# Optimization experiments

Hardware: AMD Instinct MI355X
Metric: run time of the kernel (lower is better)

Reference implementation:

```python
import jax, jax.numpy as jnp
import numpy as np

B, H, S, D = 4, 16, 4096, 64

def setup_inputs() -> dict:
    key = jax.random.key(0)
    kq, kk, kv = jax.random.split(key, 3)
    q = jax.random.normal(kq, (B, H, S, D), dtype=jnp.float32)
    k = jax.random.normal(kk, (B, H, S, D), dtype=jnp.float32)
    v = jax.random.normal(kv, (B, H, S, D), dtype=jnp.float32)
    return {"q": q, "k": k, "v": v}

def reference(q, k, v):
    # Original: (q @ k^T) @ v with score [B,H,S,S].
    # Mathematically identical reassociation: q @ (k^T @ v),
    # state kv has shape [B,H,D,D] -> avoids the SxS intermediate.
    kv = jnp.einsum('bhsd,bhse->bhde', k, v)  # [B,H,D,D]
    out = jnp.einsum('bhsd,bhde->bhse', q, kv)  # [B,H,S,D]
    return out
```

## Files before the change

### kernel.cpp

```cpp
#include <hip/hip_runtime.h>

#define BH  64
#define SEQ 4096
#define DH  64
#define NCHUNK 16
#define CROWS  (SEQ / NCHUNK)
#define KSTEPS (CROWS / 32)

typedef __attribute__((ext_vector_type(8))) short bf16x8v;
typedef __attribute__((ext_vector_type(4))) float f32x4v;

__device__ __forceinline__ short f2bf(float x) {
  unsigned u = __float_as_uint(x);
  return (short)((u + 0x7FFFu + ((u >> 16) & 1u)) >> 16);
}

__global__ __launch_bounds__(256, 4) void kv_partial_kernel(
    const float* __restrict__ k, const float* __restrict__ v,
    float* __restrict__ partial) {
  const int t = threadIdx.x;
  const int bh = blockIdx.x >> 4;
  const int chunk = blockIdx.x & (NCHUNK - 1);

  const int l  = t & 63;
  const int w  = t >> 6;
  const int lg = l >> 4;
  const int ln = l & 15;
  const int d0 = (w & 1) * 32;
  const int e0 = (w >> 1) * 32;

  const size_t sb = (size_t)bh * SEQ * DH + (size_t)chunk * CROWS * DH;
  const float* kp0 = k + sb + (size_t)(lg * 8) * DH + d0 + ln;
  const float* kp1 = kp0 + 16;
  const float* vp0 = v + sb + (size_t)(lg * 8) * DH + e0 + ln;
  const float* vp1 = vp0 + 16;

  f32x4v acc00 = {0.f, 0.f, 0.f, 0.f};
  f32x4v acc01 = acc00, acc10 = acc00, acc11 = acc00;

  float ck0[8], ck1[8], cv0[8], cv1[8];
#pragma unroll
  for (int j = 0; j < 8; ++j) {
    ck0[j] = kp0[j * DH]; ck1[j] = kp1[j * DH];
    cv0[j] = vp0[j * DH]; cv1[j] = vp1[j * DH];
  }

  for (int ks = 0; ks < KSTEPS; ++ks) {
    float nk0[8], nk1[8], nv0[8], nv1[8];
    if (ks + 1 < KSTEPS) {
      const size_t off = (size_t)(ks + 1) * 32 * DH;
#pragma unroll
      for (int j = 0; j < 8; ++j) {
        nk0[j] = kp0[off + j * DH]; nk1[j] = kp1[off + j * DH];
        nv0[j] = vp0[off + j * DH]; nv1[j] = vp1[off + j * DH];
      }
    }

    bf16x8v a0, a1, b0, b1;
#pragma unroll
    for (int j = 0; j < 8; ++j) {
      a0[j] = f2bf(ck0[j]); a1[j] = f2bf(ck1[j]);
      b0[j] = f2bf(cv0[j]); b1[j] = f2bf(cv1[j]);
    }

    acc00 = __builtin_amdgcn_mfma_f32_16x16x32_bf16(a0, b0, acc00, 0, 0, 0);
    acc01 = __builtin_amdgcn_mfma_f32_16x16x32_bf16(a0, b1, acc01, 0, 0, 0);
    acc10 = __builtin_amdgcn_mfma_f32_16x16x32_bf16(a1, b0, acc10, 0, 0, 0);
    acc11 = __builtin_amdgcn_mfma_f32_16x16x32_bf16(a1, b1, acc11, 0, 0, 0);

    if (ks + 1 < KSTEPS) {
#pragma unroll
      for (int j = 0; j < 8; ++j) {
        ck0[j] = nk0[j]; ck1[j] = nk1[j];
        cv0[j] = nv0[j]; cv1[j] = nv1[j];
      }
    }
  }

  float* pb = partial + (size_t)blockIdx.x * (DH * DH);
  const int rbase = lg * 4;
#pragma unroll
  for (int r = 0; r < 4; ++r) {
    pb[(d0 +  0 + rbase + r) * 64 + e0 +  0 + ln] = acc00[r];
    pb[(d0 +  0 + rbase + r) * 64 + e0 + 16 + ln] = acc01[r];
    pb[(d0 + 16 + rbase + r) * 64 + e0 +  0 + ln] = acc10[r];
    pb[(d0 + 16 + rbase + r) * 64 + e0 + 16 + ln] = acc11[r];
  }
}

__global__ __launch_bounds__(256) void kv_reduce_kernel(
    const float* __restrict__ partial, float* __restrict__ kvf) {
  const int gid = blockIdx.x * 256 + threadIdx.x;
  const int bh = gid >> 10;
  const int idx = gid & 1023;
  float4 s = {0.f, 0.f, 0.f, 0.f};
  for (int c = 0; c < NCHUNK; ++c) {
    const float4* p = (const float4*)(partial + ((size_t)bh * NCHUNK + c) * (DH * DH));
    float4 x = p[idx];
    s.x += x.x; s.y += x.y; s.z += x.z; s.w += x.w;
  }
  ((float4*)kvf)[gid] = s;
}

__global__ __launch_bounds__(256) void out_kernel(
    const float* __restrict__ q, const float* __restrict__ kvf,
    float* __restrict__ out) {
  const int t = threadIdx.x;
  const int bh = blockIdx.x >> 6;
  const int rb = blockIdx.x & 63;
  const int row = rb * 64 + (t >> 2);
  const int c0 = (t & 3) * 16;

  __shared__ float kv_lds[64 * 64];

  const float4* gkv4 = (const float4*)(kvf + (size_t)bh * (DH * DH));
  float4* kv4 = (float4*)kv_lds;
#pragma unroll
  for (int j = 0; j < 4; ++j) kv4[t + j * 256] = gkv4[t + j * 256];

  const float* qrow = q + (size_t)bh * SEQ * DH + (size_t)row * DH;
  float4 qv[16];
#pragma unroll
  for (int i = 0; i < 16; ++i) qv[i] = *(const float4*)&qrow[i * 4];

  __syncthreads();

  float acc[16];
#pragma unroll
  for (int j = 0; j < 16; ++j) acc[j] = 0.f;

#pragma unroll
  for (int dc = 0; dc < 16; ++dc) {
    float qs[4] = {qv[dc].x, qv[dc].y, qv[dc].z, qv[dc].w};
#pragma unroll
    for (int dd = 0; dd < 4; ++dd) {
      const float* kr = &kv_lds[(dc * 4 + dd) * 64 + c0];
      float4 k0 = *(const float4*)&kr[0];
      float4 k1 = *(const float4*)&kr[4];
      float4 k2 = *(const float4*)&kr[8];
      float4 k3 = *(const float4*)&kr[12];
      const float qsv = qs[dd];
      acc[0]  += qsv * k0.x; acc[1]  += qsv * k0.y;
      acc[2]  += qsv * k0.z; acc[3]  += qsv * k0.w;
      acc[4]  += qsv * k1.x; acc[5]  += qsv * k1.y;
      acc[6]  += qsv * k1.z; acc[7]  += qsv * k1.w;
      acc[8]  += qsv * k2.x; acc[9]  += qsv * k2.y;
      acc[10] += qsv * k2.z; acc[11] += qsv * k2.w;
      acc[12] += qsv * k3.x; acc[13] += qsv * k3.y;
      acc[14] += qsv * k3.z; acc[15] += qsv * k3.w;
    }
  }

  float* ob = out + (size_t)bh * SEQ * DH + (size_t)row * DH + c0;
#pragma unroll
  for (int j = 0; j < 4; ++j) {
    float4 w = {acc[4 * j + 0], acc[4 * j + 1], acc[4 * j + 2], acc[4 * j + 3]};
    *(float4*)&ob[4 * j] = w;
  }
}

extern "C" void kernel_launch(void* const* d_in, const int* in_sizes, int n_in,
                              void* d_out, int out_size, void* d_ws, size_t ws_size,
                              hipStream_t stream) {
  const float* q = (const float*)d_in[0];
  const float* k = (const float*)d_in[1];
  const float* v = (const float*)d_in[2];
  float* out = (float*)d_out;

  float* kvf = (float*)d_ws;
  float* partial = kvf + (size_t)BH * DH * DH;

  hipLaunchKernelGGL(kv_partial_kernel, dim3(BH * NCHUNK), dim3(256), 0, stream,
                     k, v, partial);
  hipLaunchKernelGGL(kv_reduce_kernel, dim3(256), dim3(256), 0, stream,
                     partial, kvf);
  hipLaunchKernelGGL(out_kernel, dim3(BH * 64), dim3(256), 0, stream,
                     q, kvf, out);
}
```

Baseline: 76.03 us.

## Stage K/V tiles through LDS with direct global-to-LDS loads, double-buffered

The partial K^T V kernel now copies each 32-row K and V tile into shared memory with 16-byte global_load_lds instructions and double buffering. Operands for the MFMA are then read from LDS, replacing per-lane strided scalar global loads held in registers. The goal is wider, coalesced global accesses and lower register pressure. In exchange it adds 32KB of LDS per block, which may limit occupancy, plus a barrier every iteration.

```diff
diff --git a/kernel.cpp b/kernel.cpp
--- a/kernel.cpp
+++ b/kernel.cpp
@@ -5,7 +5,7 @@
 #define DH  64
 #define NCHUNK 16
 #define CROWS  (SEQ / NCHUNK)
-#define KSTEPS (CROWS / 32)
+#define NT     (CROWS / 32)
 
 typedef __attribute__((ext_vector_type(8))) short bf16x8v;
 typedef __attribute__((ext_vector_type(4))) float f32x4v;
@@ -13,6 +13,12 @@
 __device__ __forceinline__ short f2bf(float x) {
   unsigned u = __float_as_uint(x);
   return (short)((u + 0x7FFFu + ((u >> 16) & 1u)) >> 16);
+}
+
+__device__ __forceinline__ void gload_lds16(const float* g, float* l) {
+  __builtin_amdgcn_global_load_lds(
+      (const __attribute__((address_space(1))) void*)g,
+      (__attribute__((address_space(3))) void*)l, 16, 0, 0);
 }
 
 __global__ __launch_bounds__(256, 4) void kv_partial_kernel(
@@ -29,38 +35,45 @@
   const int d0 = (w & 1) * 32;
   const int e0 = (w >> 1) * 32;
 
-  const size_t sb = (size_t)bh * SEQ * DH + (size_t)chunk * CROWS * DH;
-  const float* kp0 = k + sb + (size_t)(lg * 8) * DH + d0 + ln;
-  const float* kp1 = kp0 + 16;
-  const float* vp0 = v + sb + (size_t)(lg * 8) * DH + e0 + ln;
-  const float* vp1 = vp0 + 16;
+  const float* kb = k + (size_t)bh * SEQ * DH + (size_t)chunk * CROWS * DH;
+  const float* vb = v + (size_t)bh * SEQ * DH + (size_t)chunk * CROWS * DH;
+
+  __shared__ float smem[8192];
+
+  auto STAGE = [&](int tt) {
+    const int buf = tt & 1;
+    const size_t goff = (size_t)tt * 32 * DH;
+    const int wo = w * 256;
+#pragma unroll
+    for (int i = 0; i < 2; ++i) {
+      gload_lds16(kb + goff + i * 1024 + wo + l * 4,
+                  smem + buf * 2048 + i * 1024 + wo);
+      gload_lds16(vb + goff + i * 1024 + wo + l * 4,
+                  smem + 4096 + buf * 2048 + i * 1024 + wo);
+    }
+  };
 
   f32x4v acc00 = {0.f, 0.f, 0.f, 0.f};
   f32x4v acc01 = acc00, acc10 = acc00, acc11 = acc00;
 
-  float ck0[8], ck1[8], cv0[8], cv1[8];
-#pragma unroll
-  for (int j = 0; j < 8; ++j) {
-    ck0[j] = kp0[j * DH]; ck1[j] = kp1[j * DH];
-    cv0[j] = vp0[j * DH]; cv1[j] = vp1[j * DH];
-  }
+  STAGE(0);
+  asm volatile("s_waitcnt vmcnt(0)" ::: "memory");
+  __syncthreads();
 
-  for (int ks = 0; ks < KSTEPS; ++ks) {
-    float nk0[8], nk1[8], nv0[8], nv1[8];
-    if (ks + 1 < KSTEPS) {
-      const size_t off = (size_t)(ks + 1) * 32 * DH;
-#pragma unroll
-      for (int j = 0; j < 8; ++j) {
-        nk0[j] = kp0[off + j * DH]; nk1[j] = kp1[off + j * DH];
-        nv0[j] = vp0[off + j * DH]; nv1[j] = vp1[off + j * DH];
-      }
-    }
+  for (int tt = 0; tt < NT; ++tt) {
+    if (tt + 1 < NT) STAGE(tt + 1);
+
+    const float* ksb = smem + (tt & 1) * 2048;
+    const float* vsb = smem + 4096 + (tt & 1) * 2048;
 
     bf16x8v a0, a1, b0, b1;
 #pragma unroll
     for (int j = 0; j < 8; ++j) {
-      a0[j] = f2bf(ck0[j]); a1[j] = f2bf(ck1[j]);
-      b0[j] = f2bf(cv0[j]); b1[j] = f2bf(cv1[j]);
+      const int r = (lg * 8 + j) * 64;
+      a0[j] = f2bf(ksb[r + d0 + ln]);
+      a1[j] = f2bf(ksb[r + d0 + 16 + ln]);
+      b0[j] = f2bf(vsb[r + e0 + ln]);
+      b1[j] = f2bf(vsb[r + e0 + 16 + ln]);
     }
 
     acc00 = __builtin_amdgcn_mfma_f32_16x16x32_bf16(a0, b0, acc00, 0, 0, 0);
@@ -68,13 +81,8 @@
     acc10 = __builtin_amdgcn_mfma_f32_16x16x32_bf16(a1, b0, acc10, 0, 0, 0);
     acc11 = __builtin_amdgcn_mfma_f32_16x16x32_bf16(a1, b1, acc11, 0, 0, 0);
 
-    if (ks + 1 < KSTEPS) {
-#pragma unroll
-      for (int j = 0; j < 8; ++j) {
-        ck0[j] = nk0[j]; ck1[j] = nk1[j];
-        cv0[j] = nv0[j]; cv1[j] = nv1[j];
-      }
-    }
+    asm volatile("s_waitcnt vmcnt(0)" ::: "memory");
+    __syncthreads();
   }
 
   float* pb = partial + (size_t)blockIdx.x * (DH * DH);
```

Result: no change. 76.91 us (+1.2%).

## Replace bf16 MFMA partial KV kernel with fp32 FMA outer-product accumulation

Applied to the files above, without the earlier changes.

The k^T v partial-sum kernel drops the bf16 conversion and MFMA path. Each thread now computes a 4x4 fp32 outer-product tile, reading float4 rows of k and v for every sequence position. This removes bf16 rounding and the conversion instructions, making the result exact fp32, but moves the work onto plain vector FMAs with more, partly redundant global and cache loads per thread. The launch-bounds occupancy hint is also dropped.

```diff
diff --git a/kernel.cpp b/kernel.cpp
--- a/kernel.cpp
+++ b/kernel.cpp
@@ -5,86 +5,47 @@
 #define DH  64
 #define NCHUNK 16
 #define CROWS  (SEQ / NCHUNK)
-#define KSTEPS (CROWS / 32)
 
-typedef __attribute__((ext_vector_type(8))) short bf16x8v;
-typedef __attribute__((ext_vector_type(4))) float f32x4v;
-
-__device__ __forceinline__ short f2bf(float x) {
-  unsigned u = __float_as_uint(x);
-  return (short)((u + 0x7FFFu + ((u >> 16) & 1u)) >> 16);
-}
-
-__global__ __launch_bounds__(256, 4) void kv_partial_kernel(
+__global__ __launch_bounds__(256) void kv_partial_kernel(
     const float* __restrict__ k, const float* __restrict__ v,
     float* __restrict__ partial) {
   const int t = threadIdx.x;
   const int bh = blockIdx.x >> 4;
   const int chunk = blockIdx.x & (NCHUNK - 1);
-
   const int l  = t & 63;
   const int w  = t >> 6;
-  const int lg = l >> 4;
-  const int ln = l & 15;
-  const int d0 = (w & 1) * 32;
-  const int e0 = (w >> 1) * 32;
+  const int dg = l >> 4;
+  const int eg = l & 15;
+  const int drow = w * 16 + dg * 4;
+  const int e0 = eg * 4;
 
-  const size_t sb = (size_t)bh * SEQ * DH + (size_t)chunk * CROWS * DH;
-  const float* kp0 = k + sb + (size_t)(lg * 8) * DH + d0 + ln;
-  const float* kp1 = kp0 + 16;
-  const float* vp0 = v + sb + (size_t)(lg * 8) * DH + e0 + ln;
-  const float* vp1 = vp0 + 16;
+  const size_t base = (size_t)bh * SEQ * DH + (size_t)chunk * CROWS * DH;
+  const float* kp = k + base + drow;
+  const float* vp = v + base + e0;
 
-  f32x4v acc00 = {0.f, 0.f, 0.f, 0.f};
-  f32x4v acc01 = acc00, acc10 = acc00, acc11 = acc00;
+  float acc[4][4];
+#pragma unroll
+  for (int i = 0; i < 4; ++i)
+#pragma unroll
+    for (int j = 0; j < 4; ++j) acc[i][j] = 0.f;
 
-  float ck0[8], ck1[8], cv0[8], cv1[8];
+#pragma unroll 4
+  for (int s = 0; s < CROWS; ++s) {
+    float4 k4 = *(const float4*)(kp + (size_t)s * DH);
+    float4 v4 = *(const float4*)(vp + (size_t)s * DH);
+    float kk[4] = {k4.x, k4.y, k4.z, k4.w};
+    float vv[4] = {v4.x, v4.y, v4.z, v4.w};
 #pragma unroll
-  for (int j = 0; j < 8; ++j) {
-    ck0[j] = kp0[j * DH]; ck1[j] = kp1[j * DH];
-    cv0[j] = vp0[j * DH]; cv1[j] = vp1[j * DH];
-  }
-
-  for (int ks = 0; ks < KSTEPS; ++ks) {
-    float nk0[8], nk1[8], nv0[8], nv1[8];
-    if (ks + 1 < KSTEPS) {
-      const size_t off = (size_t)(ks + 1) * 32 * DH;
+    for (int i = 0; i < 4; ++i)
 #pragma unroll
-      for (int j = 0; j < 8; ++j) {
-        nk0[j] = kp0[off + j * DH]; nk1[j] = kp1[off + j * DH];
-        nv0[j] = vp0[off + j * DH]; nv1[j] = vp1[off + j * DH];
-      }
-    }
-
-    bf16x8v a0, a1, b0, b1;
-#pragma unroll
-    for (int j = 0; j < 8; ++j) {
-      a0[j] = f2bf(ck0[j]); a1[j] = f2bf(ck1[j]);
-      b0[j] = f2bf(cv0[j]); b1[j] = f2bf(cv1[j]);
-    }
-
-    acc00 = __builtin_amdgcn_mfma_f32_16x16x32_bf16(a0, b0, acc00, 0, 0, 0);
-    acc01 = __builtin_amdgcn_mfma_f32_16x16x32_bf16(a0, b1, acc01, 0, 0, 0);
-    acc10 = __builtin_amdgcn_mfma_f32_16x16x32_bf16(a1, b0, acc10, 0, 0, 0);
-    acc11 = __builtin_amdgcn_mfma_f32_16x16x32_bf16(a1, b1, acc11, 0, 0, 0);
-
-    if (ks + 1 < KSTEPS) {
-#pragma unroll
-      for (int j = 0; j < 8; ++j) {
-        ck0[j] = nk0[j]; ck1[j] = nk1[j];
-        cv0[j] = nv0[j]; cv1[j] = nv1[j];
-      }
-    }
+      for (int j = 0; j < 4; ++j) acc[i][j] += kk[i] * vv[j];
   }
 
   float* pb = partial + (size_t)blockIdx.x * (DH * DH);
-  const int rbase = lg * 4;
 #pragma unroll
-  for (int r = 0; r < 4; ++r) {
-    pb[(d0 +  0 + rbase + r) * 64 + e0 +  0 + ln] = acc00[r];
-    pb[(d0 +  0 + rbase + r) * 64 + e0 + 16 + ln] = acc01[r];
-    pb[(d0 + 16 + rbase + r) * 64 + e0 +  0 + ln] = acc10[r];
-    pb[(d0 + 16 + rbase + r) * 64 + e0 + 16 + ln] = acc11[r];
+  for (int i = 0; i < 4; ++i) {
+    float4 x = {acc[i][0], acc[i][1], acc[i][2], acc[i][3]};
+    *(float4*)&pb[(size_t)(drow + i) * 64 + e0] = x;
   }
 }
 
```

Measured after the change: 145.6 us. +91.5%, slower.
